# Kernel tuning notes

Measured on AMD Instinct MI355X. Metric: run time of the kernel, lower is better.

Reference implementation:

```python
import jax, jax.numpy as jnp
import numpy as np

B, T, I, H, O = 2048, 512, 1, 64, 1


def setup_inputs() -> dict:
    key = jax.random.key(0)
    ks = jax.random.split(key, 7)
    k = 1.0 / np.sqrt(H)  # PyTorch default uniform init bound
    u = lambda kk, sh: jax.random.uniform(kk, sh, jnp.float32, -k, k)
    return {
        "x": jax.random.normal(ks[0], (B, T, I), jnp.float32),
        "w_ih": u(ks[1], (4 * H, I)),   # gate order: i, f, g, o (PyTorch)
        "w_hh": u(ks[2], (4 * H, H)),
        "b_ih": u(ks[3], (4 * H,)),
        "b_hh": u(ks[4], (4 * H,)),
        "w_lin": u(ks[5], (O, H)),
        "b_lin": u(ks[6], (O,)),
    }


def _lstm_last_h(x, w_ih, w_hh, b_ih, b_hh):
    """Single-layer LSTM (PyTorch gate order i,f,g,o), returns h at the last step."""
    Bsz = x.shape[0]
    Hs = w_hh.shape[1]
    # Precompute input contribution for all timesteps: [B, T, 4H]
    gx_all = jnp.einsum('bti,gi->btg', x, w_ih) + b_ih + b_hh

    def step(carry, gx):
        h, c = carry
        g = gx + h @ w_hh.T  # [B, 4H]
        i, f, gg, o = jnp.split(g, 4, axis=-1)
        i = jax.nn.sigmoid(i)
        f = jax.nn.sigmoid(f)
        gg = jnp.tanh(gg)
        o = jax.nn.sigmoid(o)
        c = f * c + i * gg
        h = o * jnp.tanh(c)
        return (h, c), None

    h0 = jnp.zeros((Bsz, Hs), x.dtype)
    (h_last, _), _ = jax.lax.scan(step, (h0, h0), jnp.swapaxes(gx_all, 0, 1))
    return h_last  # == out[:, -1, :]


def reference(x, w_ih, w_hh, b_ih, b_hh, w_lin, b_lin):
    h = _lstm_last_h(x, w_ih, w_hh, b_ih, b_hh)
    return h @ w_lin.T + b_lin  # [B, O]
```

## Files before the change

### kernel.cpp

```cpp
#include <hip/hip_runtime.h>


typedef float    f32x4 __attribute__((ext_vector_type(4)));
typedef _Float16 f16x8 __attribute__((ext_vector_type(8)));

namespace {
constexpr int Bsz = 2048;
constexpr int Tsz = 512;
constexpr int Hsz = 64;
constexpr int NB  = 4;
}

__device__ __forceinline__ float rcp_f(float x) { return __builtin_amdgcn_rcpf(x); }
__device__ __forceinline__ float sigm(float x) {
    return rcp_f(1.0f + __expf(-x));
}
__device__ __forceinline__ float tanh_rcp(float x) {
    return fmaf(2.0f, rcp_f(1.0f + __expf(-2.0f * x)), -1.0f);
}

__global__ __launch_bounds__(256, 2)
void lstm_v4(const float* __restrict__ x,
             const float* __restrict__ w_ih,
             const float* __restrict__ w_hh,
             const float* __restrict__ b_ih,
             const float* __restrict__ b_hh,
             const float* __restrict__ w_lin,
             const float* __restrict__ b_lin,
             float* __restrict__ out)
{
    __shared__ __align__(16) float x_lds[Tsz][NB];
    __shared__ __align__(16) char  hA[16 * 128];
    __shared__ __align__(16) float g_raw[256 * NB];

    const int tid = threadIdx.x;
    const int wv  = tid >> 6;
    const int ln  = tid & 63;
    const int b0  = blockIdx.x * NB;

    #pragma unroll
    for (int it = 0; it < 2; ++it) {
        int i  = tid + it * 256;
        int b  = i >> 7;
        int t4 = i & 127;
        float4 v = reinterpret_cast<const float4*>(x + (size_t)(b0 + b) * Tsz)[t4];
        x_lds[t4 * 4 + 0][b] = v.x;
        x_lds[t4 * 4 + 1][b] = v.y;
        x_lds[t4 * 4 + 2][b] = v.z;
        x_lds[t4 * 4 + 3][b] = v.w;
    }

    const int col = ln & 15;
    const int grp = ln >> 4;

    f16x8 Wf[4][2];
    #pragma unroll
    for (int tn = 0; tn < 4; ++tn) {
        const float* wrow = w_hh + (size_t)(wv * 64 + tn * 16 + col) * Hsz;
        #pragma unroll
        for (int kc = 0; kc < 2; ++kc) {
            f16x8 w;
            #pragma unroll
            for (int e = 0; e < 8; ++e)
                w[e] = (_Float16)wrow[kc * 32 + grp * 8 + e];
            Wf[tn][kc] = w;
        }
    }

    float wih[4], bias[4];
    #pragma unroll
    for (int tn = 0; tn < 4; ++tn) {
        const int g = wv * 64 + tn * 16 + col;
        wih[tn]  = w_ih[g];
        bias[tn] = b_ih[g] + b_hh[g];
    }

    const int sw    = (col & 7) << 4;
    const int aoff0 = col * 128 + ((0 * 64 + grp * 16) ^ sw);
    const int aoff1 = col * 128 + ((1 * 64 + grp * 16) ^ sw);

    const int pb = tid & 3;
    const int pj = tid >> 2;
    const float wlin  = w_lin[pj];
    const float blin0 = b_lin[0];
    const int hwoff = pb * 128 + ((2 * pj) ^ (pb << 4));

    reinterpret_cast<float2*>(hA)[tid] = make_float2(0.0f, 0.0f);

    float c = 0.0f, h = 0.0f;

    __syncthreads();

    for (int t = 0; t < Tsz; ++t) {
        const float4 xb = *(const float4*)&x_lds[t][0];
        f16x8 A0 = *(const f16x8*)(hA + aoff0);
        f16x8 A1 = *(const f16x8*)(hA + aoff1);

        f32x4 acc[4];
        #pragma unroll
        for (int tn = 0; tn < 4; ++tn) {
            acc[tn][0] = fmaf(xb.x, wih[tn], bias[tn]);
            acc[tn][1] = fmaf(xb.y, wih[tn], bias[tn]);
            acc[tn][2] = fmaf(xb.z, wih[tn], bias[tn]);
            acc[tn][3] = fmaf(xb.w, wih[tn], bias[tn]);
        }

        #pragma unroll
        for (int tn = 0; tn < 4; ++tn)
            acc[tn] = __builtin_amdgcn_mfma_f32_16x16x32_f16(A0, Wf[tn][0], acc[tn], 0, 0, 0);
        #pragma unroll
        for (int tn = 0; tn < 4; ++tn)
            acc[tn] = __builtin_amdgcn_mfma_f32_16x16x32_f16(A1, Wf[tn][1], acc[tn], 0, 0, 0);

        if (ln < 16) {
            #pragma unroll
            for (int tn = 0; tn < 4; ++tn)
                *(f32x4*)&g_raw[(wv * 64 + tn * 16 + ln) * 4] = acc[tn];
        }
        __syncthreads();

        const float gi = g_raw[tid +   0];
        const float gf = g_raw[tid + 256];
        const float gg = g_raw[tid + 512];
        const float go = g_raw[tid + 768];

        const float ig = sigm(gi);
        const float fg = sigm(gf);
        const float tg = tanh_rcp(gg);
        const float og = sigm(go);

        c = fmaf(fg, c, ig * tg);
        h = og * tanh_rcp(c);

        *(_Float16*)(hA + hwoff) = (_Float16)h;

        __syncthreads();
    }

    float p = h * wlin;
    #pragma unroll
    for (int off = 4; off < 64; off <<= 1)
        p += __shfl_xor(p, off, 64);
    if (ln < 4) g_raw[wv * 4 + ln] = p;
    __syncthreads();
    if (tid < 4)
        out[b0 + tid] = g_raw[tid] + g_raw[4 + tid] +
                        g_raw[8 + tid] + g_raw[12 + tid] + blin0;
}

extern "C" void kernel_launch(void* const* d_in, const int* in_sizes, int n_in,
                              void* d_out, int out_size, void* d_ws, size_t ws_size,
                              hipStream_t stream) {
    const float* x     = (const float*)d_in[0];
    const float* w_ih  = (const float*)d_in[1];
    const float* w_hh  = (const float*)d_in[2];
    const float* b_ih  = (const float*)d_in[3];
    const float* b_hh  = (const float*)d_in[4];
    const float* w_lin = (const float*)d_in[5];
    const float* b_lin = (const float*)d_in[6];
    float* out = (float*)d_out;

    dim3 grid(Bsz / NB);
    dim3 block(256);
    lstm_v4<<<grid, block, 0, stream>>>(x, w_ih, w_hh, b_ih, b_hh,
                                        w_lin, b_lin, out);
}
```

Baseline: 281.1 us.

## Halve batch per block, raise occupancy, fold exp scale into weights

Each block now handles 2 batch rows instead of 4, so the grid doubles to 1024 blocks and launch bounds allow 4 blocks per CU. The goal is more concurrent blocks to hide the latency of the serial timestep chain. The -log2e and -2log2e gate scales are folded into the f16 weights, input weights and biases, so the activations use raw exp2 and rcp. The trade-off is that half the MFMA tile rows are wasted, only 128 threads do gate math, and scaling before the f16 cast slightly changes rounding.

```diff
diff --git a/kernel.cpp b/kernel.cpp
--- a/kernel.cpp
+++ b/kernel.cpp
@@ -7,20 +7,20 @@
 namespace {
 constexpr int Bsz = 2048;
 constexpr int Tsz = 512;
-constexpr int Hsz = 64;
-constexpr int NB  = 4;
+constexpr int NBW = 2;
 }
 
-__device__ __forceinline__ float rcp_f(float x) { return __builtin_amdgcn_rcpf(x); }
-__device__ __forceinline__ float sigm(float x) {
-    return rcp_f(1.0f + __expf(-x));
-}
-__device__ __forceinline__ float tanh_rcp(float x) {
-    return fmaf(2.0f, rcp_f(1.0f + __expf(-2.0f * x)), -1.0f);
+__device__ __forceinline__ float rcp_f(float v)  { return __builtin_amdgcn_rcpf(v); }
+__device__ __forceinline__ float exp2_f(float v) { return __builtin_amdgcn_exp2f(v); }
+
+__device__ __forceinline__ float sigm_s(float gs)  { return rcp_f(1.0f + exp2_f(gs)); }
+__device__ __forceinline__ float tanh_s(float gs)  { return fmaf(2.0f, rcp_f(1.0f + exp2_f(gs)), -1.0f); }
+__device__ __forceinline__ float tanh_plain(float v) {
+    return fmaf(2.0f, rcp_f(1.0f + exp2_f(v * -2.88539008178f)), -1.0f);
 }
 
-__global__ __launch_bounds__(256, 2)
-void lstm_v4(const float* __restrict__ x,
+__global__ __launch_bounds__(256, 4)
+void lstm_v7(const float* __restrict__ x,
              const float* __restrict__ w_ih,
              const float* __restrict__ w_hh,
              const float* __restrict__ b_ih,
@@ -29,82 +29,77 @@
              const float* __restrict__ b_lin,
              float* __restrict__ out)
 {
-    __shared__ __align__(16) float x_lds[Tsz][NB];
+    __shared__ __align__(16) float x_lds[Tsz][NBW];
     __shared__ __align__(16) char  hA[16 * 128];
-    __shared__ __align__(16) float g_raw[256 * NB];
+    __shared__ __align__(16) float g_raw[256 * NBW];
+    __shared__ float part[2 * NBW];
 
     const int tid = threadIdx.x;
     const int wv  = tid >> 6;
     const int ln  = tid & 63;
-    const int b0  = blockIdx.x * NB;
+    const int col = ln & 15;
+    const int grp = ln >> 4;
+    const int b0  = blockIdx.x * NBW;
 
-    #pragma unroll
-    for (int it = 0; it < 2; ++it) {
-        int i  = tid + it * 256;
-        int b  = i >> 7;
-        int t4 = i & 127;
-        float4 v = reinterpret_cast<const float4*>(x + (size_t)(b0 + b) * Tsz)[t4];
+    constexpr float LOG2E = 1.44269504089f;
+    const float s = (wv == 2) ? (-2.0f * LOG2E) : (-LOG2E);
+
+    {
+        const int b  = tid >> 7;
+        const int t4 = tid & 127;
+        const float4 v = ((const float4*)(x + (size_t)(b0 + b) * Tsz))[t4];
         x_lds[t4 * 4 + 0][b] = v.x;
         x_lds[t4 * 4 + 1][b] = v.y;
         x_lds[t4 * 4 + 2][b] = v.z;
         x_lds[t4 * 4 + 3][b] = v.w;
     }
 
-    const int col = ln & 15;
-    const int grp = ln >> 4;
-
     f16x8 Wf[4][2];
+    float wihc[4], biasc[4];
     #pragma unroll
     for (int tn = 0; tn < 4; ++tn) {
-        const float* wrow = w_hh + (size_t)(wv * 64 + tn * 16 + col) * Hsz;
+        const int gate = wv * 64 + tn * 16 + col;
+        const float* wrow = w_hh + (size_t)gate * 64;
         #pragma unroll
         for (int kc = 0; kc < 2; ++kc) {
             f16x8 w;
             #pragma unroll
             for (int e = 0; e < 8; ++e)
-                w[e] = (_Float16)wrow[kc * 32 + grp * 8 + e];
+                w[e] = (_Float16)(wrow[kc * 32 + grp * 8 + e] * s);
             Wf[tn][kc] = w;
         }
-    }
-
-    float wih[4], bias[4];
-    #pragma unroll
-    for (int tn = 0; tn < 4; ++tn) {
-        const int g = wv * 64 + tn * 16 + col;
-        wih[tn]  = w_ih[g];
-        bias[tn] = b_ih[g] + b_hh[g];
+        wihc[tn]  = w_ih[gate] * s;
+        biasc[tn] = (b_ih[gate] + b_hh[gate]) * s;
     }
 
     const int sw    = (col & 7) << 4;
-    const int aoff0 = col * 128 + ((0 * 64 + grp * 16) ^ sw);
-    const int aoff1 = col * 128 + ((1 * 64 + grp * 16) ^ sw);
+    const int aoff0 = col * 128 + ((grp * 16) ^ sw);
+    const int aoff1 = col * 128 + ((64 + grp * 16) ^ sw);
 
-    const int pb = tid & 3;
-    const int pj = tid >> 2;
+    const int pb = tid & 1;
+    const int pj = (tid >> 1) & 63;
     const float wlin  = w_lin[pj];
-    const float blin0 = b_lin[0];
-    const int hwoff = pb * 128 + ((2 * pj) ^ (pb << 4));
+    const int   hwoff = pb * 128 + ((2 * pj) ^ (pb << 4));
 
-    reinterpret_cast<float2*>(hA)[tid] = make_float2(0.0f, 0.0f);
+    ((float2*)hA)[tid] = make_float2(0.0f, 0.0f);
 
     float c = 0.0f, h = 0.0f;
 
     __syncthreads();
 
     for (int t = 0; t < Tsz; ++t) {
-        const float4 xb = *(const float4*)&x_lds[t][0];
-        f16x8 A0 = *(const f16x8*)(hA + aoff0);
-        f16x8 A1 = *(const f16x8*)(hA + aoff1);
+        const float2 xb = *(const float2*)&x_lds[t][0];
+        const f16x8 A0 = *(const f16x8*)(hA + aoff0);
+        const f16x8 A1 = *(const f16x8*)(hA + aoff1);
 
         f32x4 acc[4];
         #pragma unroll
         for (int tn = 0; tn < 4; ++tn) {
-            acc[tn][0] = fmaf(xb.x, wih[tn], bias[tn]);
-            acc[tn][1] = fmaf(xb.y, wih[tn], bias[tn]);
-            acc[tn][2] = fmaf(xb.z, wih[tn], bias[tn]);
-            acc[tn][3] = fmaf(xb.w, wih[tn], bias[tn]);
+            acc[tn][0] = fmaf(xb.x, wihc[tn], biasc[tn]);
+            acc[tn][1] = fmaf(xb.y, wihc[tn], biasc[tn]);
+            acc[tn][2] = biasc[tn];
+            acc[tn][3] = biasc[tn];
         }
-
         #pragma unroll
         for (int tn = 0; tn < 4; ++tn)
             acc[tn] = __builtin_amdgcn_mfma_f32_16x16x32_f16(A0, Wf[tn][0], acc[tn], 0, 0, 0);
@@ -114,38 +109,43 @@
 
         if (ln < 16) {
             #pragma unroll
-            for (int tn = 0; tn < 4; ++tn)
-                *(f32x4*)&g_raw[(wv * 64 + tn * 16 + ln) * 4] = acc[tn];
+            for (int tn = 0; tn < 4; ++tn) {
+                float2 gw;
+                gw.x = acc[tn][0];
+                gw.y = acc[tn][1];
+                *(float2*)&g_raw[(wv * 64 + tn * 16 + ln) * 2] = gw;
+            }
         }
         __syncthreads();
 
-        const float gi = g_raw[tid +   0];
-        const float gf = g_raw[tid + 256];
-        const float gg = g_raw[tid + 512];
-        const float go = g_raw[tid + 768];
+        if (tid < 128) {
+            const float gi = g_raw[tid +   0];
+            const float gf = g_raw[tid + 128];
+            const float gg = g_raw[tid + 256];
+            const float go = g_raw[tid + 384];
 
-        const float ig = sigm(gi);
-        const float fg = sigm(gf);
-        const float tg = tanh_rcp(gg);
-        const float og = sigm(go);
+            const float ig = sigm_s(gi);
+            const float fg = sigm_s(gf);
+            const float tg = tanh_s(gg);
+            const float og = sigm_s(go);
+            c = fmaf(fg, c, ig * tg);
+            h = og * tanh_plain(c);
 
-        c = fmaf(fg, c, ig * tg);
-        h = og * tanh_rcp(c);
-
-        *(_Float16*)(hA + hwoff) = (_Float16)h;
-
+            *(_Float16*)(hA + hwoff) = (_Float16)h;
+        }
         __syncthreads();
     }
 
-    float p = h * wlin;
-    #pragma unroll
-    for (int off = 4; off < 64; off <<= 1)
-        p += __shfl_xor(p, off, 64);
-    if (ln < 4) g_raw[wv * 4 + ln] = p;
+    if (tid < 128) {
+        float p = h * wlin;
+        #pragma unroll
+        for (int off = 2; off < 64; off <<= 1)
+            p += __shfl_xor(p, off, 64);
+        if (ln < 2) part[wv * 2 + ln] = p;
+    }
     __syncthreads();
-    if (tid < 4)
-        out[b0 + tid] = g_raw[tid] + g_raw[4 + tid] +
-                        g_raw[8 + tid] + g_raw[12 + tid] + blin0;
+    if (tid < NBW)
+        out[b0 + tid] = part[tid] + part[2 + tid] + b_lin[0];
 }
 
 extern "C" void kernel_launch(void* const* d_in, const int* in_sizes, int n_in,
@@ -160,8 +160,8 @@
     const float* b_lin = (const float*)d_in[6];
     float* out = (float*)d_out;
 
-    dim3 grid(Bsz / NB);
+    dim3 grid(Bsz / NBW);
     dim3 block(256);
-    lstm_v4<<<grid, block, 0, stream>>>(x, w_ih, w_hh, b_ih, b_hh,
+    lstm_v7<<<grid, block, 0, stream>>>(x, w_ih, w_hh, b_ih, b_hh,
                                         w_lin, b_lin, out);
 }
```

Measured after the change: 347.4 us. 23.6% more time.
